# Optimization experiments

Hardware: AMD Instinct MI355X
Metric: run time of the kernel (lower is better)

## Reference

```python
import jax, jax.numpy as jnp
import numpy as np

N, E, B = 20000, 640000, 4096
IN_DIM, HID, A, D, C = 128, 256, 8, 64, 2


def setup_inputs() -> dict:
    key = jax.random.key(0)
    ks = jax.random.split(key, 16)
    inp = {
        "feature": jax.random.normal(ks[0], (N, IN_DIM), dtype=jnp.float32),
        "src": jax.random.randint(ks[1], (E,), 0, N),
        "dst": jax.random.randint(ks[2], (E,), 0, N),
        "pairs": jax.random.randint(ks[3], (B, 2), 0, N),
        # gcn1.linear: in_dim -> hid
        "W1": jax.random.normal(ks[4], (HID, IN_DIM), dtype=jnp.float32) * 0.02,
        "b1": jnp.zeros((HID,), dtype=jnp.float32),
        # aspEmbed (no bias): hid -> A*D
        "aspW": jax.random.normal(ks[5], (A * D, HID), dtype=jnp.float32) * 0.02,
        # Aspect_Representation.linear: D -> 1
        "attW": jax.random.normal(ks[6], (1, D), dtype=jnp.float32) * 0.02,
        "attb": jnp.zeros((1,), dtype=jnp.float32),
        # aspect_merge_linear: D -> 1
        "mergeW": jax.random.normal(ks[7], (1, D), dtype=jnp.float32) * 0.02,
        "mergeb": jnp.zeros((1,), dtype=jnp.float32),
        # concat_linear: 2A -> C
        "catW": jax.random.normal(ks[8], (C, 2 * A), dtype=jnp.float32) * 0.02,
        "catb": jnp.zeros((C,), dtype=jnp.float32),
    }
    return inp


def _aspect_head(pe, aspW, attW, attb, mergeW, mergeb):
    # pe: [B, HID]
    b = pe.shape[0]
    asp = (pe @ aspW.T).reshape(b, A, D)               # [B, A, D]
    score = jax.nn.softmax(asp @ attW.T + attb, axis=1)  # [B, A, 1] softmax over aspects
    rep = score * asp                                   # [B, A, D]
    return (rep @ mergeW.T + mergeb)[..., 0]            # [B, A]


def reference(feature, src, dst, pairs, W1, b1, aspW, attW, attb,
              mergeW, mergeb, catW, catb):
    n = feature.shape[0]
    nf = feature + feature.mean(axis=0)                 # node_feature
    # GCNLayer: u_mul_v message + mean aggregation at dst
    msg = nf[src] * nf[dst]                             # [E, IN_DIM]
    agg = jax.ops.segment_sum(msg, dst, num_segments=n)
    deg = jax.ops.segment_sum(jnp.ones((msg.shape[0],), dtype=feature.dtype), dst, num_segments=n)
    x = agg / jnp.where(deg > 0, deg, 1.0)[:, None]
    x = x @ W1.T + b1                                   # [N, HID] (dropout = identity in eval)
    p1 = _aspect_head(x[pairs[:, 0]], aspW, attW, attb, mergeW, mergeb)
    p2 = _aspect_head(x[pairs[:, 1]], aspW, attW, attb, mergeW, mergeb)
    out = jnp.concatenate([p1, p2], axis=1) @ catW.T + catb  # [B, C]
    return jax.nn.log_softmax(out, axis=-1)
```

## Files before the change

kernel.cpp:

```cpp
#include <hip/hip_runtime.h>
#include <hip/hip_bf16.h>

constexpr int IN_DIM = 128;
constexpr int HID    = 256;
constexpr int A_     = 8;
constexpr int D_     = 64;
constexpr int PAD    = 128;
constexpr int CS_ROWS = 16;

__global__ void k1_prep_zero(const float* __restrict__ aspW, const float* __restrict__ attW,
                             const float* __restrict__ mergeW, const float* __restrict__ b1,
                             const float* __restrict__ attb, const float* __restrict__ W1,
                             float* __restrict__ WS, float* __restrict__ WM,
                             float* __restrict__ sb, float* __restrict__ mb,
                             ulonglong2* __restrict__ zbase, int n16) {
  if (blockIdx.x >= A_) {
    int i = (blockIdx.x - A_) * blockDim.x + threadIdx.x;
    int stride = (gridDim.x - A_) * blockDim.x;
    ulonglong2 z; z.x = 0ull; z.y = 0ull;
    for (; i < n16; i += stride) zbase[i] = z;
    return;
  }
  __shared__ float Us[HID], Um[HID];
  __shared__ float r1[HID], r2[HID];
  int a = blockIdx.x;
  int h = threadIdx.x;
  float ss = 0.f, sm = 0.f;
  const float* ap = aspW + (size_t)(a * D_) * HID + h;
#pragma unroll 8
  for (int d = 0; d < D_; ++d) {
    float w = ap[(size_t)d * HID];
    ss += attW[d] * w;
    sm += mergeW[d] * w;
  }
  Us[h] = ss;
  Um[h] = sm;
  float bv = b1[h];
  r1[h] = ss * bv;
  r2[h] = sm * bv;
  __syncthreads();
  for (int ofs = HID / 2; ofs > 0; ofs >>= 1) {
    if (h < ofs) { r1[h] += r1[h + ofs]; r2[h] += r2[h + ofs]; }
    __syncthreads();
  }
  if (h == 0) { sb[a] = r1[0] + attb[0]; mb[a] = r2[0]; }
  __syncthreads();
  int j = h & 127, half = h >> 7;
  float ws = 0.f, wm = 0.f;
  const float* w1p = W1 + (size_t)(half * 128) * IN_DIM + j;
  const float* usp = Us + half * 128;
  const float* ump = Um + half * 128;
#pragma unroll 16
  for (int k = 0; k < 128; ++k) {
    float w = w1p[(size_t)k * IN_DIM];
    ws += usp[k] * w;
    wm += ump[k] * w;
  }
  r1[h] = ws;
  r2[h] = wm;
  __syncthreads();
  if (h < IN_DIM) {
    WS[a * IN_DIM + h] = r1[h] + r1[h + 128];
    WM[a * IN_DIM + h] = r2[h] + r2[h + 128];
  }
}

__global__ void k2_colsum_mask(const float* __restrict__ f, float* __restrict__ pb, int N,
                               int npart, const int* __restrict__ pairs,
                               int* __restrict__ mask, int* __restrict__ wl,
                               int* __restrict__ wlcnt, int nIdx) {
  if ((int)blockIdx.x >= npart) {
    int i = ((int)blockIdx.x - npart) * blockDim.x + threadIdx.x;
    if (i < nIdx) {
      int node = pairs[i];
      if (atomicCAS(&mask[node], 0, 1) == 0) {
        int p = atomicAdd(wlcnt, 1);
        wl[p] = node;
      }
    }
    return;
  }
  __shared__ float sm[8][IN_DIM];
  int tid = threadIdx.x;
  int c4  = tid & 31;
  int r   = tid >> 5;
  int base = blockIdx.x * CS_ROWS;
  float4 acc = make_float4(0.f, 0.f, 0.f, 0.f);
#pragma unroll
  for (int it = 0; it < CS_ROWS / 8; ++it) {
    int row = base + it * 8 + r;
    if (row < N) {
      float4 v = ((const float4*)f)[(size_t)row * 32 + c4];
      acc.x += v.x; acc.y += v.y; acc.z += v.z; acc.w += v.w;
    }
  }
  ((float4*)sm[r])[c4] = acc;
  __syncthreads();
  if (tid < IN_DIM) {
    float s = 0.f;
#pragma unroll
    for (int rr = 0; rr < 8; ++rr) s += sm[rr][tid];
    pb[(size_t)blockIdx.x * IN_DIM + tid] = s;
  }
}

__global__ void k3_fill_colred(const int4* __restrict__ src4, const int4* __restrict__ dst4,
                               const int* __restrict__ mask, int* __restrict__ cnt,
                               int* __restrict__ esrc, int E4, int fillBlocks,
                               const float* __restrict__ pb, float* __restrict__ colsum,
                               int npart) {
  if ((int)blockIdx.x >= fillBlocks) {
    int rblk = (int)blockIdx.x - fillBlocks;
    int t = threadIdx.x;
    float4 acc = make_float4(0.f, 0.f, 0.f, 0.f);
    for (int row = t; row < npart; row += 256) {
      float4 v = ((const float4*)(pb + (size_t)row * IN_DIM))[rblk];
      acc.x += v.x; acc.y += v.y; acc.z += v.z; acc.w += v.w;
    }
    __shared__ float4 red[256];
    red[t] = acc;
    __syncthreads();
    for (int ofs = 128; ofs > 0; ofs >>= 1) {
      if (t < ofs) {
        float4 o = red[t + ofs];
        red[t].x += o.x; red[t].y += o.y; red[t].z += o.z; red[t].w += o.w;
      }
      __syncthreads();
    }
    if (t == 0) ((float4*)colsum)[rblk] = red[0];
    return;
  }
  int e = blockIdx.x * blockDim.x + threadIdx.x;
  if (e >= E4) return;
  int4 d = dst4[e];
  int4 s = src4[e];
  if (mask[d.x]) { int p = atomicAdd(&cnt[d.x], 1); if (p < PAD) esrc[(size_t)d.x * PAD + p] = s.x; }
  if (mask[d.y]) { int p = atomicAdd(&cnt[d.y], 1); if (p < PAD) esrc[(size_t)d.y * PAD + p] = s.y; }
  if (mask[d.z]) { int p = atomicAdd(&cnt[d.z], 1); if (p < PAD) esrc[(size_t)d.z * PAD + p] = s.z; }
  if (mask[d.w]) { int p = atomicAdd(&cnt[d.w], 1); if (p < PAD) esrc[(size_t)d.w * PAD + p] = s.w; }
}

__global__ void __launch_bounds__(64) pull_k(
    const float* __restrict__ feat, const float* __restrict__ colsum,
    const int* __restrict__ cnt, const int* __restrict__ esrc,
    const int* __restrict__ wl, const int* __restrict__ wlcnt,
    const float* __restrict__ WS, const float* __restrict__ WM,
    float* __restrict__ nodevals, float invN) {
  int widx = blockIdx.x;
  if (widx >= *wlcnt) return;
  int d = wl[widx];
  int lane = threadIdx.x;
  int deg = cnt[d];
  const float2* F = (const float2*)feat;
  const int* es = esrc + (size_t)d * PAD;
  int n = deg < PAD ? deg : PAD;
  float2 acc = make_float2(0.f, 0.f);
  for (int base = 0; base < n; base += 64) {
    int rem = n - base;
    int cnt64 = rem < 64 ? rem : 64;
    int idx = (lane < cnt64) ? es[base + lane] : 0;
    int j = 0;
    for (; j + 7 < cnt64; j += 8) {
      int s0 = __shfl(idx, j + 0);
      int s1 = __shfl(idx, j + 1);
      int s2 = __shfl(idx, j + 2);
      int s3 = __shfl(idx, j + 3);
      int s4 = __shfl(idx, j + 4);
      int s5 = __shfl(idx, j + 5);
      int s6 = __shfl(idx, j + 6);
      int s7 = __shfl(idx, j + 7);
      float2 v0 = F[(size_t)s0 * 64 + lane];
      float2 v1 = F[(size_t)s1 * 64 + lane];
      float2 v2 = F[(size_t)s2 * 64 + lane];
      float2 v3 = F[(size_t)s3 * 64 + lane];
      float2 v4 = F[(size_t)s4 * 64 + lane];
      float2 v5 = F[(size_t)s5 * 64 + lane];
      float2 v6 = F[(size_t)s6 * 64 + lane];
      float2 v7 = F[(size_t)s7 * 64 + lane];
      acc.x += ((v0.x + v1.x) + (v2.x + v3.x)) + ((v4.x + v5.x) + (v6.x + v7.x));
      acc.y += ((v0.y + v1.y) + (v2.y + v3.y)) + ((v4.y + v5.y) + (v6.y + v7.y));
    }
    for (; j < cnt64; ++j) {
      int s0 = __shfl(idx, j);
      float2 v0 = F[(size_t)s0 * 64 + lane];
      acc.x += v0.x;
      acc.y += v0.y;
    }
  }
  float2 cm = ((const float2*)colsum)[lane];
  cm.x *= invN;
  cm.y *= invN;
  float2 fd = F[(size_t)d * 64 + lane];
  float2 x;
  if (deg > 0) {
    float inv = 1.0f / (float)deg;
    x.x = (fd.x + cm.x) * (acc.x * inv + cm.x);
    x.y = (fd.y + cm.y) * (acc.y * inv + cm.y);
  } else {
    x.x = 0.f;
    x.y = 0.f;
  }
  float v[16];
#pragma unroll
  for (int a = 0; a < A_; ++a) {
    float2 w = ((const float2*)WS)[a * 64 + lane];
    float2 u = ((const float2*)WM)[a * 64 + lane];
    v[a] = x.x * w.x + x.y * w.y;
    v[8 + a] = x.x * u.x + x.y * u.y;
  }
#pragma unroll
  for (int m = 32; m > 0; m >>= 1) {
#pragma unroll
    for (int k = 0; k < 16; ++k) v[k] += __shfl_xor(v[k], m, 64);
  }
  if (lane == 0) {
#pragma unroll
    for (int k = 0; k < 16; ++k) nodevals[(size_t)d * 16 + k] = v[k];
  }
}

__global__ void pair_k(const int* __restrict__ pairs, const float* __restrict__ nodevals,
                       const float* __restrict__ sb, const float* __restrict__ mb,
                       const float* __restrict__ catW, const float* __restrict__ catb,
                       const float* __restrict__ mergeb, float* __restrict__ out, int B) {
  int b = blockIdx.x * blockDim.x + threadIdx.x;
  if (b >= B) return;
  float mgb = mergeb[0];
  float p[2 * A_];
  for (int side = 0; side < 2; ++side) {
    int node = pairs[b * 2 + side];
    const float4* nv = (const float4*)(nodevals + (size_t)node * 16);
    float4 q0 = nv[0], q1 = nv[1], q2 = nv[2], q3 = nv[3];
    float s[A_] = {q0.x, q0.y, q0.z, q0.w, q1.x, q1.y, q1.z, q1.w};
    float m[A_] = {q2.x, q2.y, q2.z, q2.w, q3.x, q3.y, q3.z, q3.w};
#pragma unroll
    for (int a = 0; a < A_; ++a) { s[a] += sb[a]; m[a] += mb[a]; }
    float mx = s[0];
#pragma unroll
    for (int a = 1; a < A_; ++a) mx = fmaxf(mx, s[a]);
    float es[A_], sum = 0.f;
#pragma unroll
    for (int a = 0; a < A_; ++a) { es[a] = __expf(s[a] - mx); sum += es[a]; }
    float rsum = 1.0f / sum;
#pragma unroll
    for (int a = 0; a < A_; ++a) p[side * A_ + a] = es[a] * rsum * m[a] + mgb;
  }
  float o0 = catb[0], o1 = catb[1];
#pragma unroll
  for (int k = 0; k < 2 * A_; ++k) {
    o0 += p[k] * catW[k];
    o1 += p[k] * catW[2 * A_ + k];
  }
  float mx = fmaxf(o0, o1);
  float lse = mx + logf(__expf(o0 - mx) + __expf(o1 - mx));
  out[b * 2 + 0] = o0 - lse;
  out[b * 2 + 1] = o1 - lse;
}

extern "C" void kernel_launch(void* const* d_in, const int* in_sizes, int n_in,
                              void* d_out, int out_size, void* d_ws, size_t ws_size,
                              hipStream_t stream) {
  const float* feature = (const float*)d_in[0];
  const int*   src     = (const int*)d_in[1];
  const int*   dst     = (const int*)d_in[2];
  const int*   pairs   = (const int*)d_in[3];
  const float* W1      = (const float*)d_in[4];
  const float* b1      = (const float*)d_in[5];
  const float* aspW    = (const float*)d_in[6];
  const float* attW    = (const float*)d_in[7];
  const float* attb    = (const float*)d_in[8];
  const float* mergeW  = (const float*)d_in[9];
  const float* mergebp = (const float*)d_in[10];
  const float* catW    = (const float*)d_in[11];
  const float* catb    = (const float*)d_in[12];

  const int N = in_sizes[0] / IN_DIM;
  const int E = in_sizes[1];
  const int B = in_sizes[3] / 2;
  const int npart = (N + CS_ROWS - 1) / CS_ROWS;
  const int maskBlocks = (2 * B + 255) / 256;
  const int fillBlocks = (E / 4 + 255) / 256;
  const int E4 = E / 4;

  char* ws = (char*)d_ws;
  size_t off_b = 0;
  int* cnt = (int*)(ws + off_b);        off_b += (size_t)N * sizeof(int);
  int* mask = (int*)(ws + off_b);       off_b += (size_t)N * sizeof(int);
  int* wlcnt = (int*)(ws + off_b);      off_b += 4 * sizeof(int);
  size_t zero_bytes = (off_b + 15) & ~(size_t)15;
  off_b = zero_bytes;
  float* colsum = (float*)(ws + off_b); off_b += IN_DIM * sizeof(float);
  float* pb = (float*)(ws + off_b);     off_b += (size_t)npart * IN_DIM * sizeof(float);
  int* wl = (int*)(ws + off_b);         off_b += (size_t)(2 * B) * sizeof(int);
  float* WS = (float*)(ws + off_b);     off_b += A_ * IN_DIM * sizeof(float);
  float* WM = (float*)(ws + off_b);     off_b += A_ * IN_DIM * sizeof(float);
  float* sb = (float*)(ws + off_b);     off_b += A_ * sizeof(float);
  float* mb = (float*)(ws + off_b);     off_b += A_ * sizeof(float);
  float* nodevals = (float*)(ws + off_b); off_b += (size_t)N * 16 * sizeof(float);
  int* esrc = (int*)(ws + off_b);       off_b += (size_t)N * PAD * sizeof(int);

  k1_prep_zero<<<A_ + 40, 256, 0, stream>>>(aspW, attW, mergeW, b1, attb, W1,
                                            WS, WM, sb, mb,
                                            (ulonglong2*)d_ws, (int)(zero_bytes / 16));
  k2_colsum_mask<<<npart + maskBlocks, 256, 0, stream>>>(feature, pb, N, npart,
                                                         pairs, mask, wl, wlcnt, 2 * B);
  k3_fill_colred<<<fillBlocks + 32, 256, 0, stream>>>((const int4*)src, (const int4*)dst,
                                                      mask, cnt, esrc, E4, fillBlocks,
                                                      pb, colsum, npart);
  pull_k<<<2 * B, 64, 0, stream>>>(feature, colsum, cnt, esrc, wl, wlcnt, WS, WM,
                                   nodevals, 1.0f / (float)N);
  pair_k<<<(B + 255) / 256, 256, 0, stream>>>(pairs, nodevals, sb, mb, catW, catb,
                                              mergebp, (float*)d_out, B);
}
```

Before: 58.10 us.

## Fuse five-kernel pipeline into one cooperative persistent kernel with grid syncs

Replaces the chain of five kernel launches with a single cooperative kernel of 256 blocks by 1024 threads. Phases (weight prep, zeroing, colsum, mask/worklist, edge fill, gather-pull, pair head) are separated by grid.sync(). The aim is to remove launch gaps and inter-kernel drain costs. In exchange it gives up the finer-grained parallelism of the per-node 64-thread pull blocks, pays four grid barriers, and keeps the old multi-kernel path as a fallback if the cooperative launch fails.

```diff
diff --git a/kernel.cpp b/kernel.cpp
--- a/kernel.cpp
+++ b/kernel.cpp
@@ -1,5 +1,8 @@
 #include <hip/hip_runtime.h>
 #include <hip/hip_bf16.h>
+#include <hip/hip_cooperative_groups.h>
+
+namespace cg = cooperative_groups;
 
 constexpr int IN_DIM = 128;
 constexpr int HID    = 256;
@@ -7,6 +10,259 @@
 constexpr int D_     = 64;
 constexpr int PAD    = 128;
 constexpr int CS_ROWS = 16;
+constexpr int NBLK = 256;
+constexpr int NTHR = 1024;
+constexpr int NPART = 240;
+
+struct MegaP {
+  const float* feature; const int* src; const int* dst; const int* pairs;
+  const float* W1; const float* b1; const float* aspW; const float* attW;
+  const float* attb; const float* mergeW; const float* mergeb;
+  const float* catW; const float* catb;
+  float* out;
+  int N, E4, B;
+  int* cnt; int* mask; int* wlcnt; int* wl;
+  float* colsum; float* pb; float* WS; float* WM; float* sb; float* mb;
+  float* nodevals; int* esrc;
+  ulonglong2* zbase; int n16;
+  float invN;
+};
+
+__global__ __launch_bounds__(NTHR, 4) void mega_k(MegaP P) {
+  cg::grid_group grid = cg::this_grid();
+  __shared__ float4 smem4[1024];
+  float* smem = (float*)smem4;
+  const int bid = blockIdx.x;
+  const int t = threadIdx.x;
+
+  if (bid < A_) {
+    int a = bid;
+    float* psS = smem;
+    float* psM = smem + 1024;
+    float* Us  = smem + 2048;
+    float* Um  = smem + 2304;
+    float* r1  = smem + 2560;
+    float* r2  = smem + 2816;
+    {
+      int h = t & 255, dq = t >> 8;
+      float ss = 0.f, sm = 0.f;
+      const float* ap = P.aspW + (size_t)(a * D_ + dq * 16) * HID + h;
+#pragma unroll
+      for (int d = 0; d < 16; ++d) {
+        float w = ap[(size_t)d * HID];
+        ss += P.attW[dq * 16 + d] * w;
+        sm += P.mergeW[dq * 16 + d] * w;
+      }
+      psS[dq * 256 + h] = ss;
+      psM[dq * 256 + h] = sm;
+    }
+    __syncthreads();
+    if (t < HID) {
+      float us = psS[t] + psS[256 + t] + psS[512 + t] + psS[768 + t];
+      float um = psM[t] + psM[256 + t] + psM[512 + t] + psM[768 + t];
+      Us[t] = us; Um[t] = um;
+      float bv = P.b1[t];
+      r1[t] = us * bv; r2[t] = um * bv;
+    }
+    __syncthreads();
+    for (int ofs = 128; ofs > 0; ofs >>= 1) {
+      if (t < ofs) { r1[t] += r1[t + ofs]; r2[t] += r2[t + ofs]; }
+      __syncthreads();
+    }
+    if (t == 0) { P.sb[a] = r1[0] + P.attb[0]; P.mb[a] = r2[0]; }
+    __syncthreads();
+    {
+      int j = t & 127, ch = t >> 7;
+      float ws = 0.f, wm = 0.f;
+      const float* w1p = P.W1 + (size_t)(ch * 32) * IN_DIM + j;
+      const float* usp = Us + ch * 32;
+      const float* ump = Um + ch * 32;
+#pragma unroll
+      for (int k = 0; k < 32; ++k) {
+        float w = w1p[(size_t)k * IN_DIM];
+        ws += usp[k] * w;
+        wm += ump[k] * w;
+      }
+      psS[ch * 128 + j] = ws;
+      psM[ch * 128 + j] = wm;
+    }
+    __syncthreads();
+    if (t < IN_DIM) {
+      float ws = 0.f, wm = 0.f;
+#pragma unroll
+      for (int c = 0; c < 8; ++c) { ws += psS[c * 128 + t]; wm += psM[c * 128 + t]; }
+      P.WS[a * IN_DIM + t] = ws;
+      P.WM[a * IN_DIM + t] = wm;
+    }
+  } else if (bid < 16) {
+    ulonglong2 z; z.x = 0ull; z.y = 0ull;
+    for (int i = (bid - 8) * NTHR + t; i < P.n16; i += 8 * NTHR) P.zbase[i] = z;
+  } else {
+    int cb = bid - 16;
+    int rslot = t >> 5, c4 = t & 31;
+    float4 acc = make_float4(0.f, 0.f, 0.f, 0.f);
+    for (int row = cb * 32 + rslot; row < P.N; row += NPART * 32) {
+      float4 v = ((const float4*)P.feature)[(size_t)row * 32 + c4];
+      acc.x += v.x; acc.y += v.y; acc.z += v.z; acc.w += v.w;
+    }
+    smem4[rslot * 32 + c4] = acc;
+    __syncthreads();
+    if (t < IN_DIM) {
+      float s = 0.f;
+#pragma unroll 8
+      for (int r = 0; r < 32; ++r) s += smem[r * 128 + t];
+      P.pb[(size_t)cb * IN_DIM + t] = s;
+    }
+  }
+  grid.sync();
+
+  if (bid < 8) {
+    for (int i = bid * NTHR + t; i < 2 * P.B; i += 8 * NTHR) {
+      int node = P.pairs[i];
+      if (atomicCAS(&P.mask[node], 0, 1) == 0) {
+        int q = atomicAdd(P.wlcnt, 1);
+        P.wl[q] = node;
+      }
+    }
+  } else if (bid < 40) {
+    int c4 = bid - 8;
+    float4 acc = make_float4(0.f, 0.f, 0.f, 0.f);
+    for (int r = t; r < NPART; r += NTHR) {
+      float4 v = ((const float4*)P.pb)[(size_t)r * 32 + c4];
+      acc.x += v.x; acc.y += v.y; acc.z += v.z; acc.w += v.w;
+    }
+    smem4[t] = acc;
+    __syncthreads();
+    for (int ofs = 512; ofs > 0; ofs >>= 1) {
+      if (t < ofs) {
+        float4 o = smem4[t + ofs], m = smem4[t];
+        m.x += o.x; m.y += o.y; m.z += o.z; m.w += o.w;
+        smem4[t] = m;
+      }
+      __syncthreads();
+    }
+    if (t == 0) ((float4*)P.colsum)[c4] = smem4[0];
+  }
+  grid.sync();
+
+  for (int e = bid * NTHR + t; e < P.E4; e += NBLK * NTHR) {
+    int4 d4 = ((const int4*)P.dst)[e];
+    int4 s4 = ((const int4*)P.src)[e];
+    if (P.mask[d4.x]) { int q = atomicAdd(&P.cnt[d4.x], 1); if (q < PAD) P.esrc[(size_t)d4.x * PAD + q] = s4.x; }
+    if (P.mask[d4.y]) { int q = atomicAdd(&P.cnt[d4.y], 1); if (q < PAD) P.esrc[(size_t)d4.y * PAD + q] = s4.y; }
+    if (P.mask[d4.z]) { int q = atomicAdd(&P.cnt[d4.z], 1); if (q < PAD) P.esrc[(size_t)d4.z * PAD + q] = s4.z; }
+    if (P.mask[d4.w]) { int q = atomicAdd(&P.cnt[d4.w], 1); if (q < PAD) P.esrc[(size_t)d4.w * PAD + q] = s4.w; }
+  }
+  grid.sync();
+
+  {
+    int wln = __hip_atomic_load(P.wlcnt, __ATOMIC_RELAXED, __HIP_MEMORY_SCOPE_AGENT);
+    int lane = t & 63;
+    int wg = bid * (NTHR / 64) + (t >> 6);
+    const float2* F = (const float2*)P.feature;
+    float2 cm = ((const float2*)P.colsum)[lane];
+    cm.x *= P.invN; cm.y *= P.invN;
+    float2 wsv[A_], wmv[A_];
+#pragma unroll
+    for (int a = 0; a < A_; ++a) {
+      wsv[a] = ((const float2*)P.WS)[a * 64 + lane];
+      wmv[a] = ((const float2*)P.WM)[a * 64 + lane];
+    }
+    for (int widx = wg; widx < wln; widx += NBLK * (NTHR / 64)) {
+      int d = P.wl[widx];
+      int deg = P.cnt[d];
+      const int* es = P.esrc + (size_t)d * PAD;
+      int n = deg < PAD ? deg : PAD;
+      float2 acc = make_float2(0.f, 0.f);
+      for (int base = 0; base < n; base += 64) {
+        int rem = n - base;
+        int cnt64 = rem < 64 ? rem : 64;
+        int idx = (lane < cnt64) ? es[base + lane] : 0;
+        int j = 0;
+        for (; j + 7 < cnt64; j += 8) {
+          int s0 = __shfl(idx, j + 0), s1 = __shfl(idx, j + 1);
+          int s2 = __shfl(idx, j + 2), s3 = __shfl(idx, j + 3);
+          int s4 = __shfl(idx, j + 4), s5 = __shfl(idx, j + 5);
+          int s6 = __shfl(idx, j + 6), s7 = __shfl(idx, j + 7);
+          float2 v0 = F[(size_t)s0 * 64 + lane];
+          float2 v1 = F[(size_t)s1 * 64 + lane];
+          float2 v2 = F[(size_t)s2 * 64 + lane];
+          float2 v3 = F[(size_t)s3 * 64 + lane];
+          float2 v4 = F[(size_t)s4 * 64 + lane];
+          float2 v5 = F[(size_t)s5 * 64 + lane];
+          float2 v6 = F[(size_t)s6 * 64 + lane];
+          float2 v7 = F[(size_t)s7 * 64 + lane];
+          acc.x += ((v0.x + v1.x) + (v2.x + v3.x)) + ((v4.x + v5.x) + (v6.x + v7.x));
+          acc.y += ((v0.y + v1.y) + (v2.y + v3.y)) + ((v4.y + v5.y) + (v6.y + v7.y));
+        }
+        for (; j < cnt64; ++j) {
+          int s0 = __shfl(idx, j);
+          float2 v0 = F[(size_t)s0 * 64 + lane];
+          acc.x += v0.x;
+          acc.y += v0.y;
+        }
+      }
+      float2 fd = F[(size_t)d * 64 + lane];
+      float2 x;
+      if (deg > 0) {
+        float inv = 1.0f / (float)deg;
+        x.x = (fd.x + cm.x) * (acc.x * inv + cm.x);
+        x.y = (fd.y + cm.y) * (acc.y * inv + cm.y);
+      } else {
+        x.x = 0.f; x.y = 0.f;
+      }
+      float v[16];
+#pragma unroll
+      for (int a = 0; a < A_; ++a) {
+        v[a]     = x.x * wsv[a].x + x.y * wsv[a].y;
+        v[8 + a] = x.x * wmv[a].x + x.y * wmv[a].y;
+      }
+#pragma unroll
+      for (int m = 32; m > 0; m >>= 1) {
+#pragma unroll
+        for (int k = 0; k < 16; ++k) v[k] += __shfl_xor(v[k], m, 64);
+      }
+      if (lane == 0) {
+#pragma unroll
+        for (int k = 0; k < 16; ++k) P.nodevals[(size_t)d * 16 + k] = v[k];
+      }
+    }
+  }
+  grid.sync();
+
+  for (int g = bid * NTHR + t; g < P.B; g += NBLK * NTHR) {
+    float mgb = P.mergeb[0];
+    float pp[2 * A_];
+    for (int side = 0; side < 2; ++side) {
+      int node = P.pairs[g * 2 + side];
+      const float4* nv = (const float4*)(P.nodevals + (size_t)node * 16);
+      float4 q0 = nv[0], q1 = nv[1], q2 = nv[2], q3 = nv[3];
+      float s[A_] = {q0.x, q0.y, q0.z, q0.w, q1.x, q1.y, q1.z, q1.w};
+      float m[A_] = {q2.x, q2.y, q2.z, q2.w, q3.x, q3.y, q3.z, q3.w};
+#pragma unroll
+      for (int a = 0; a < A_; ++a) { s[a] += P.sb[a]; m[a] += P.mb[a]; }
+      float mx = s[0];
+#pragma unroll
+      for (int a = 1; a < A_; ++a) mx = fmaxf(mx, s[a]);
+      float es[A_], sum = 0.f;
+#pragma unroll
+      for (int a = 0; a < A_; ++a) { es[a] = __expf(s[a] - mx); sum += es[a]; }
+      float rsum = 1.0f / sum;
+#pragma unroll
+      for (int a = 0; a < A_; ++a) pp[side * A_ + a] = es[a] * rsum * m[a] + mgb;
+    }
+    float o0 = P.catb[0], o1 = P.catb[1];
+#pragma unroll
+    for (int k = 0; k < 2 * A_; ++k) {
+      o0 += pp[k] * P.catW[k];
+      o1 += pp[k] * P.catW[2 * A_ + k];
+    }
+    float mx = fmaxf(o0, o1);
+    float lse = mx + logf(__expf(o0 - mx) + __expf(o1 - mx));
+    P.out[g * 2 + 0] = o0 - lse;
+    P.out[g * 2 + 1] = o1 - lse;
+  }
+}
 
 __global__ void k1_prep_zero(const float* __restrict__ aspW, const float* __restrict__ attW,
                              const float* __restrict__ mergeW, const float* __restrict__ b1,
@@ -161,14 +417,10 @@
     int idx = (lane < cnt64) ? es[base + lane] : 0;
     int j = 0;
     for (; j + 7 < cnt64; j += 8) {
-      int s0 = __shfl(idx, j + 0);
-      int s1 = __shfl(idx, j + 1);
-      int s2 = __shfl(idx, j + 2);
-      int s3 = __shfl(idx, j + 3);
-      int s4 = __shfl(idx, j + 4);
-      int s5 = __shfl(idx, j + 5);
-      int s6 = __shfl(idx, j + 6);
-      int s7 = __shfl(idx, j + 7);
+      int s0 = __shfl(idx, j + 0), s1 = __shfl(idx, j + 1);
+      int s2 = __shfl(idx, j + 2), s3 = __shfl(idx, j + 3);
+      int s4 = __shfl(idx, j + 4), s5 = __shfl(idx, j + 5);
+      int s6 = __shfl(idx, j + 6), s7 = __shfl(idx, j + 7);
       float2 v0 = F[(size_t)s0 * 64 + lane];
       float2 v1 = F[(size_t)s1 * 64 + lane];
       float2 v2 = F[(size_t)s2 * 64 + lane];
@@ -277,7 +529,7 @@
   const int N = in_sizes[0] / IN_DIM;
   const int E = in_sizes[1];
   const int B = in_sizes[3] / 2;
-  const int npart = (N + CS_ROWS - 1) / CS_ROWS;
+  const int npart_fb = (N + CS_ROWS - 1) / CS_ROWS;
   const int maskBlocks = (2 * B + 255) / 256;
   const int fillBlocks = (E / 4 + 255) / 256;
   const int E4 = E / 4;
@@ -290,7 +542,7 @@
   size_t zero_bytes = (off_b + 15) & ~(size_t)15;
   off_b = zero_bytes;
   float* colsum = (float*)(ws + off_b); off_b += IN_DIM * sizeof(float);
-  float* pb = (float*)(ws + off_b);     off_b += (size_t)npart * IN_DIM * sizeof(float);
+  float* pb = (float*)(ws + off_b);     off_b += (size_t)npart_fb * IN_DIM * sizeof(float);
   int* wl = (int*)(ws + off_b);         off_b += (size_t)(2 * B) * sizeof(int);
   float* WS = (float*)(ws + off_b);     off_b += A_ * IN_DIM * sizeof(float);
   float* WM = (float*)(ws + off_b);     off_b += A_ * IN_DIM * sizeof(float);
@@ -299,16 +551,34 @@
   float* nodevals = (float*)(ws + off_b); off_b += (size_t)N * 16 * sizeof(float);
   int* esrc = (int*)(ws + off_b);       off_b += (size_t)N * PAD * sizeof(int);
 
-  k1_prep_zero<<<A_ + 40, 256, 0, stream>>>(aspW, attW, mergeW, b1, attb, W1,
-                                            WS, WM, sb, mb,
-                                            (ulonglong2*)d_ws, (int)(zero_bytes / 16));
-  k2_colsum_mask<<<npart + maskBlocks, 256, 0, stream>>>(feature, pb, N, npart,
-                                                         pairs, mask, wl, wlcnt, 2 * B);
-  k3_fill_colred<<<fillBlocks + 32, 256, 0, stream>>>((const int4*)src, (const int4*)dst,
-                                                      mask, cnt, esrc, E4, fillBlocks,
-                                                      pb, colsum, npart);
-  pull_k<<<2 * B, 64, 0, stream>>>(feature, colsum, cnt, esrc, wl, wlcnt, WS, WM,
-                                   nodevals, 1.0f / (float)N);
-  pair_k<<<(B + 255) / 256, 256, 0, stream>>>(pairs, nodevals, sb, mb, catW, catb,
-                                              mergebp, (float*)d_out, B);
-}
+  MegaP P;
+  P.feature = feature; P.src = src; P.dst = dst; P.pairs = pairs;
+  P.W1 = W1; P.b1 = b1; P.aspW = aspW; P.attW = attW; P.attb = attb;
+  P.mergeW = mergeW; P.mergeb = mergebp; P.catW = catW; P.catb = catb;
+  P.out = (float*)d_out;
+  P.N = N; P.E4 = E4; P.B = B;
+  P.cnt = cnt; P.mask = mask; P.wlcnt = wlcnt; P.wl = wl;
+  P.colsum = colsum; P.pb = pb; P.WS = WS; P.WM = WM; P.sb = sb; P.mb = mb;
+  P.nodevals = nodevals; P.esrc = esrc;
+  P.zbase = (ulonglong2*)d_ws; P.n16 = (int)(zero_bytes / 16);
+  P.invN = 1.0f / (float)N;
+
+  void* args[] = {&P};
+  hipError_t err = hipLaunchCooperativeKernel((const void*)mega_k, dim3(NBLK),
+                                              dim3(NTHR), args, 0, stream);
+  if (err != hipSuccess) {
+    (void)hipGetLastError();
+    k1_prep_zero<<<A_ + 40, 256, 0, stream>>>(aspW, attW, mergeW, b1, attb, W1,
+                                              WS, WM, sb, mb,
+                                              (ulonglong2*)d_ws, (int)(zero_bytes / 16));
+    k2_colsum_mask<<<npart_fb + maskBlocks, 256, 0, stream>>>(feature, pb, N, npart_fb,
+                                                              pairs, mask, wl, wlcnt, 2 * B);
+    k3_fill_colred<<<fillBlocks + 32, 256, 0, stream>>>((const int4*)src, (const int4*)dst,
+                                                        mask, cnt, esrc, E4, fillBlocks,
+                                                        pb, colsum, npart_fb);
+    pull_k<<<2 * B, 64, 0, stream>>>(feature, colsum, cnt, esrc, wl, wlcnt, WS, WM,
+                                     nodevals, 1.0f / (float)N);
+    pair_k<<<(B + 255) / 256, 256, 0, stream>>>(pairs, nodevals, sb, mb, catW, catb,
+                                                mergebp, (float*)d_out, B);
+  }
+}
```

Result: slower. 180.5 us (+210.7%).
